# Kernel optimization log

Hardware: AMD Instinct MI355X
Metric: run time of the kernel (lower is better)

The kernel has to match this reference:

```python
import jax, jax.numpy as jnp
import numpy as np
from itertools import product

C_IN, C_OUT = 32, 64
N_DOWN = 100000
CHILD = 4
N = N_DOWN * CHILD  # 400000 active voxels


def _encode(c):
    # pack nonnegative (x,y,z) voxel coords into a single int64 key
    c = c.astype(np.int64)
    return (c[:, 0] << 40) | (c[:, 1] << 20) | c[:, 2]


def _build_coords(rng):
    # N_DOWN unique parent voxels in [1,126]^3, each with exactly CHILD distinct children
    flat = rng.choice(126 ** 3, N_DOWN, replace=False)
    px = flat // (126 * 126) + 1
    py = (flat // 126) % 126 + 1
    pz = flat % 126 + 1
    parents = np.stack([px, py, pz], 1)  # [N_DOWN,3]
    child_off = rng.random((N_DOWN, 8)).argsort(1)[:, :CHILD]  # [N_DOWN,4] in 0..7
    bits = np.stack([child_off >> 2 & 1, child_off >> 1 & 1, child_off & 1], -1)  # [N_DOWN,4,3]
    children = (2 * parents[:, None, :] + bits).reshape(N, 3)
    kvec = child_off.reshape(N)  # kernel offset id of each child within its parent
    parent_of = np.repeat(np.arange(N_DOWN), CHILD)
    return children, kvec, parent_of


def _build_kmap3(children):
    # submanifold 3x3x3 neighbor map: km_in[k,i] = index j with coords[j] = coords[i] + off_k
    keys = _encode(children)
    order = np.argsort(keys)
    skeys = keys[order]
    offsets = list(product((-1, 0, 1), repeat=3))
    km_in = np.full((27, N), N, np.int32)
    km_out = np.full((27, N), N, np.int32)
    ar = np.arange(N, dtype=np.int32)
    for k, off in enumerate(offsets):
        nk = _encode(children + np.asarray(off))
        pos = np.clip(np.searchsorted(skeys, nk), 0, N - 1)
        found = skeys[pos] == nk
        km_in[k] = np.where(found, order[pos].astype(np.int32), N)
        km_out[k] = np.where(found, ar, N)
    return km_in, km_out


def _build_kmap_pool(kvec, parent_of):
    # kernel-2 stride-2 conv: each child feeds exactly one parent at offset kvec
    kp_in = np.full((8, N), N, np.int32)
    kp_out = np.full((8, N), N_DOWN, np.int32)
    for k in range(8):
        idx = np.nonzero(kvec == k)[0]
        kp_in[k, :len(idx)] = idx
        kp_out[k, :len(idx)] = parent_of[idx]
    return kp_in, kp_out


def setup_inputs() -> dict:
    rng = np.random.default_rng(0)
    children, kvec, parent_of = _build_coords(rng)
    km_in, km_out = _build_kmap3(children)
    kp_in, kp_out = _build_kmap_pool(kvec, parent_of)

    key = jax.random.key(0)
    ks = jax.random.split(key, 10)
    f32 = jnp.float32
    return {
        'x': jax.random.normal(ks[0], (N, C_IN), f32),
        'W1': jax.random.normal(ks[1], (27, C_IN, C_OUT), f32) * 0.05,
        'bn1_s': jax.random.uniform(ks[2], (C_OUT,), f32, 0.5, 1.5),
        'bn1_b': jax.random.normal(ks[3], (C_OUT,), f32) * 0.1,
        'W2': jax.random.normal(ks[4], (27, C_OUT, C_OUT), f32) * 0.05,
        'bn2_s': jax.random.uniform(ks[5], (C_OUT,), f32, 0.5, 1.5),
        'bn2_b': jax.random.normal(ks[6], (C_OUT,), f32) * 0.1,
        'Wp': jax.random.normal(ks[7], (8, C_OUT, C_OUT), f32) * 0.05,
        'bnp_s': jax.random.uniform(ks[8], (C_OUT,), f32, 0.5, 1.5),
        'bnp_b': jax.random.normal(ks[9], (C_OUT,), f32) * 0.1,
        'km_in': jnp.asarray(km_in),
        'km_out': jnp.asarray(km_out),
        'kp_in': jnp.asarray(kp_in),
        'kp_out': jnp.asarray(kp_out),
        'n_down': N_DOWN,
    }


def _sparse_conv(x, W, iidx, oidx, n_out):
    # gather -> per-offset matmul -> scatter-add; invalid pairs point at zero row / dump row
    xp = jnp.concatenate([x, jnp.zeros((1, x.shape[1]), x.dtype)], 0)
    def body(acc, a):
        Wk, ii, oi = a
        return acc.at[oi].add(xp[ii] @ Wk), None
    acc0 = jnp.zeros((n_out + 1, W.shape[2]), x.dtype)
    acc, _ = jax.lax.scan(body, acc0, (W, iidx, oidx))
    return acc[:n_out]


def _bn_relu(h, s, b):
    return jax.nn.relu(h * s + b)


def reference(x, W1, bn1_s, bn1_b, W2, bn2_s, bn2_b, Wp, bnp_s, bnp_b,
              km_in, km_out, kp_in, kp_out, n_down):
    n = x.shape[0]
    h = _bn_relu(_sparse_conv(x, W1, km_in, km_out, n), bn1_s, bn1_b)
    down = _bn_relu(_sparse_conv(h, W2, km_in, km_out, n), bn2_s, bn2_b)
    p = _bn_relu(_sparse_conv(down, Wp, kp_in, kp_out, n_down), bnp_s, bnp_b)
    return (down, p)
```

## Files before the change

kernel.cpp:

```cpp
#include <hip/hip_runtime.h>


#define NV 400000
#define ND 100000

typedef __attribute__((ext_vector_type(8))) short  bf16x8;
typedef __attribute__((ext_vector_type(4))) float  f32x4;

__device__ __forceinline__ unsigned short f2b(float f) {
    unsigned int u = __builtin_bit_cast(unsigned int, f);
    u += 0x7fffu + ((u >> 16) & 1u);
    return (unsigned short)(u >> 16);
}

__global__ __launch_bounds__(256) void cvt_bf16_k(
    const float* __restrict__ in, unsigned short* __restrict__ out, int n)
{
    int t = (blockIdx.x * 256 + threadIdx.x) * 4;
    if (t >= n) return;
    float4 f = *(const float4*)(in + t);
    ushort4 u;
    u.x = f2b(f.x); u.y = f2b(f.y); u.z = f2b(f.z); u.w = f2b(f.w);
    *(ushort4*)(out + t) = u;
}

__global__ __launch_bounds__(256) void pack_w_k(
    const float* __restrict__ W, unsigned short* __restrict__ out, int nk, int ci)
{
    int t = blockIdx.x * 256 + threadIdx.x;
    int steps = ci >> 5;
    if (t >= nk * steps * 4 * 64) return;
    int lane = t & 63;
    int nt   = (t >> 6) & 3;
    int rest = t >> 8;
    int s    = rest % steps;
    int k    = rest / steps;
    int col = lane & 15, quad = lane >> 4;
    int co = nt * 16 + col;
    unsigned short v[8];
#pragma unroll
    for (int j = 0; j < 8; ++j) {
        int cidx = s * 32 + quad * 8 + j;
        v[j] = f2b(W[((size_t)k * ci + cidx) * 64 + co]);
    }
    bf16x8 frag;
#pragma unroll
    for (int j = 0; j < 8; ++j) frag[j] = (short)v[j];
    *(bf16x8*)(out + (size_t)t * 8) = frag;
}

__global__ __launch_bounds__(256) void ck_init_k(int* __restrict__ ck)
{
    int t = blockIdx.x * 256 + threadIdx.x;
    if (t < ND * 8) ck[t] = NV;
}
__global__ __launch_bounds__(256) void ck_scatter_k(
    const int* __restrict__ kp_in, const int* __restrict__ kp_out,
    int* __restrict__ ck)
{
    int t = blockIdx.x * 256 + threadIdx.x;
    if (t >= 8 * NV) return;
    int j = kp_in[t];
    if (j == NV) return;
    int k = t / NV;
    ck[(size_t)k * ND + kp_out[t]] = j;
}

template <int CI, int NK, int MODE, int NR>
__global__ __launch_bounds__(256) void conv_mfma(
    const unsigned short* __restrict__ xin,
    const unsigned short* __restrict__ Wp,
    const int* __restrict__ km,
    const float* __restrict__ bns, const float* __restrict__ bnb,
    float* __restrict__ outf, unsigned short* __restrict__ outb)
{
    constexpr int STEPS = CI / 32;
    constexpr int FR = STEPS * 4;
    __shared__ unsigned short bsh[2 * FR * 512];

    const int lane = threadIdx.x & 63;
    const int wave = threadIdx.x >> 6;
    const int col = lane & 15, quad = lane >> 4;

    const int nwg = gridDim.x;
    const int q = nwg >> 3, r = nwg & 7;
    const int xcd = blockIdx.x & 7, bodd = blockIdx.x >> 3;
    const int bid = (xcd < r ? xcd * (q + 1) : r * (q + 1) + (xcd - r) * q) + bodd;

    const int wbase = (bid * 4 + wave) * 64;

    int rowm[4];
#pragma unroll
    for (int mt = 0; mt < 4; ++mt) {
        int rr = wbase + mt * 16 + col;
        rowm[mt] = rr < NR ? rr : NR - 1;
    }

    f32x4 acc[4][4];
#pragma unroll
    for (int mt = 0; mt < 4; ++mt)
#pragma unroll
        for (int nt = 0; nt < 4; ++nt) acc[mt][nt] = (f32x4)0.f;

    auto stage = [&](int k, int b) {
#pragma unroll
        for (int f = wave; f < FR; f += 4) {
            const unsigned short* src = Wp + ((size_t)(k * FR + f) * 64 + lane) * 8;
            __builtin_amdgcn_global_load_lds(
                (const __attribute__((address_space(1))) void*)src,
                (__attribute__((address_space(3))) void*)&bsh[b * (FR * 512) + f * 512],
                16, 0, 0);
        }
    };

    stage(0, 0);
    int buf = 0;

    for (int k = 0; k < NK; ++k) {
        __syncthreads();
        if (k + 1 < NK) stage(k + 1, buf ^ 1);

        const int* __restrict__ kmr = km + (size_t)k * NR;
        int j[4];
#pragma unroll
        for (int mt = 0; mt < 4; ++mt) j[mt] = kmr[rowm[mt]];

#pragma unroll
        for (int s = 0; s < STEPS; ++s) {
            bf16x8 a[4];
#pragma unroll
            for (int mt = 0; mt < 4; ++mt)
                a[mt] = *(const bf16x8*)(xin + (size_t)j[mt] * CI + s * 32 + quad * 8);
#pragma unroll
            for (int nt = 0; nt < 4; ++nt) {
                bf16x8 b = *(const bf16x8*)&bsh[buf * (FR * 512) + (s * 4 + nt) * 512 + lane * 8];
#pragma unroll
                for (int mt = 0; mt < 4; ++mt)
                    acc[mt][nt] = __builtin_amdgcn_mfma_f32_16x16x32_bf16(
                        a[mt], b, acc[mt][nt], 0, 0, 0);
            }
        }
        buf ^= 1;
    }

#pragma unroll
    for (int nt = 0; nt < 4; ++nt) {
        const int n = nt * 16 + col;
        const float sc = bns[n], bi = bnb[n];
#pragma unroll
        for (int mt = 0; mt < 4; ++mt)
#pragma unroll
            for (int rr = 0; rr < 4; ++rr) {
                int row = wbase + mt * 16 + quad * 4 + rr;
                if (row < NR) {
                    float v = fmaxf(fmaf(acc[mt][nt][rr], sc, bi), 0.f);
                    if constexpr (MODE == 0) {
                        outf[(size_t)row * 64 + n] = v;
                    } else if constexpr (MODE == 1) {
                        outb[(size_t)row * 64 + n] = f2b(v);
                    } else {
                        outf[(size_t)row * 64 + n] = v;
                        outb[(size_t)row * 64 + n] = f2b(v);
                    }
                }
            }
    }
}

extern "C" void kernel_launch(void* const* d_in, const int* in_sizes, int n_in,
                              void* d_out, int out_size, void* d_ws, size_t ws_size,
                              hipStream_t stream)
{
    const float* x    = (const float*)d_in[0];
    const float* W1   = (const float*)d_in[1];
    const float* bn1s = (const float*)d_in[2];
    const float* bn1b = (const float*)d_in[3];
    const float* W2   = (const float*)d_in[4];
    const float* bn2s = (const float*)d_in[5];
    const float* bn2b = (const float*)d_in[6];
    const float* Wp   = (const float*)d_in[7];
    const float* bnps = (const float*)d_in[8];
    const float* bnpb = (const float*)d_in[9];
    const int* km_in  = (const int*)d_in[10];
    const int* kp_in  = (const int*)d_in[12];
    const int* kp_out = (const int*)d_in[13];

    float* down = (float*)d_out;
    float* pout = (float*)d_out + (size_t)NV * 64;

    char* ws = (char*)d_ws;
    unsigned short* x_bf  = (unsigned short*)ws;  ws += (size_t)(NV + 1) * 32 * 2;
    unsigned short* h_bf  = (unsigned short*)ws;  ws += (size_t)(NV + 1) * 64 * 2;
    unsigned short* d_bf  = (unsigned short*)ws;  ws += (size_t)(NV + 1) * 64 * 2;
    int*            ck    = (int*)ws;             ws += (size_t)8 * ND * 4;
    unsigned short* W1p   = (unsigned short*)ws;  ws += (size_t)27 * 32 * 64 * 2;
    unsigned short* W2p   = (unsigned short*)ws;  ws += (size_t)27 * 64 * 64 * 2;
    unsigned short* Wpp   = (unsigned short*)ws;

    hipMemsetAsync(x_bf + (size_t)NV * 32, 0, 32 * 2, stream);
    hipMemsetAsync(h_bf + (size_t)NV * 64, 0, 64 * 2, stream);
    hipMemsetAsync(d_bf + (size_t)NV * 64, 0, 64 * 2, stream);

    cvt_bf16_k<<<(NV * 32 / 4 + 255) / 256, 256, 0, stream>>>(x, x_bf, NV * 32);
    pack_w_k<<<(27 * 1 * 4 * 64 + 255) / 256, 256, 0, stream>>>(W1, W1p, 27, 32);
    pack_w_k<<<(27 * 2 * 4 * 64 + 255) / 256, 256, 0, stream>>>(W2, W2p, 27, 64);
    pack_w_k<<<(8  * 2 * 4 * 64 + 255) / 256, 256, 0, stream>>>(Wp, Wpp, 8, 64);
    ck_init_k<<<(ND * 8 + 255) / 256, 256, 0, stream>>>(ck);
    ck_scatter_k<<<(8 * NV + 255) / 256, 256, 0, stream>>>(kp_in, kp_out, ck);

    const int cgrid = (NV + 255) / 256;
    conv_mfma<32, 27, 1, NV><<<cgrid, 256, 0, stream>>>(
        x_bf, W1p, km_in, bn1s, bn1b, nullptr, h_bf);
    conv_mfma<64, 27, 2, NV><<<cgrid, 256, 0, stream>>>(
        h_bf, W2p, km_in, bn2s, bn2b, down, d_bf);
    conv_mfma<64, 8, 0, ND><<<(ND + 255) / 256, 256, 0, stream>>>(
        d_bf, Wpp, ck, bnps, bnpb, pout, nullptr);
}
```

Baseline: 587.1 us.

## Skip empty neighbor tiles per wave and load weights directly from global

```diff
diff --git a/kernel.cpp b/kernel.cpp
--- a/kernel.cpp
+++ b/kernel.cpp
@@ -75,9 +75,6 @@
     float* __restrict__ outf, unsigned short* __restrict__ outb)
 {
     constexpr int STEPS = CI / 32;
-    constexpr int FR = STEPS * 4;
-    __shared__ unsigned short bsh[2 * FR * 512];
-
     const int lane = threadIdx.x & 63;
     const int wave = threadIdx.x >> 6;
     const int col = lane & 15, quad = lane >> 4;
@@ -102,45 +99,38 @@
 #pragma unroll
         for (int nt = 0; nt < 4; ++nt) acc[mt][nt] = (f32x4)0.f;
 
-    auto stage = [&](int k, int b) {
-#pragma unroll
-        for (int f = wave; f < FR; f += 4) {
-            const unsigned short* src = Wp + ((size_t)(k * FR + f) * 64 + lane) * 8;
-            __builtin_amdgcn_global_load_lds(
-                (const __attribute__((address_space(1))) void*)src,
-                (__attribute__((address_space(3))) void*)&bsh[b * (FR * 512) + f * 512],
-                16, 0, 0);
-        }
-    };
-
-    stage(0, 0);
-    int buf = 0;
-
     for (int k = 0; k < NK; ++k) {
-        __syncthreads();
-        if (k + 1 < NK) stage(k + 1, buf ^ 1);
-
         const int* __restrict__ kmr = km + (size_t)k * NR;
         int j[4];
 #pragma unroll
         for (int mt = 0; mt < 4; ++mt) j[mt] = kmr[rowm[mt]];
 
+        int live[4];
+#pragma unroll
+        for (int mt = 0; mt < 4; ++mt)
+            live[mt] = __builtin_amdgcn_readfirstlane((int)__any(j[mt] != NV));
+        if (!(live[0] | live[1] | live[2] | live[3])) continue;
+
 #pragma unroll
         for (int s = 0; s < STEPS; ++s) {
-            bf16x8 a[4];
-#pragma unroll
-            for (int mt = 0; mt < 4; ++mt)
-                a[mt] = *(const bf16x8*)(xin + (size_t)j[mt] * CI + s * 32 + quad * 8);
-#pragma unroll
-            for (int nt = 0; nt < 4; ++nt) {
-                bf16x8 b = *(const bf16x8*)&bsh[buf * (FR * 512) + (s * 4 + nt) * 512 + lane * 8];
-#pragma unroll
-                for (int mt = 0; mt < 4; ++mt)
-                    acc[mt][nt] = __builtin_amdgcn_mfma_f32_16x16x32_bf16(
-                        a[mt], b, acc[mt][nt], 0, 0, 0);
+            const unsigned short* bp =
+                Wp + ((((size_t)k * STEPS + s) * 4) * 64 + lane) * 8;
+            bf16x8 b[4];
+#pragma unroll
+            for (int nt = 0; nt < 4; ++nt)
+                b[nt] = *(const bf16x8*)(bp + (size_t)nt * 512);
+#pragma unroll
+            for (int mt = 0; mt < 4; ++mt) {
+                if (live[mt]) {
+                    bf16x8 a = *(const bf16x8*)(
+                        xin + (size_t)j[mt] * CI + s * 32 + quad * 8);
+#pragma unroll
+                    for (int nt = 0; nt < 4; ++nt)
+                        acc[mt][nt] = __builtin_amdgcn_mfma_f32_16x16x32_bf16(
+                            a, b[nt], acc[mt][nt], 0, 0, 0);
+                }
             }
         }
-        buf ^= 1;
     }
 
 #pragma unroll
```

Result: slower. 730.3 us (+24.4%).
